# Kernel optimization log

Hardware: AMD Instinct MI355X
Metric: run time of the kernel (lower is better)

The kernel has to match this reference:

```python
import jax, jax.numpy as jnp
import numpy as np

WS = (7, 7)          # window size
SS = (3, 3)          # shift size
HP, WP = 112, 112    # patch grid H, W
C = 128              # embedding dim
NH = 8               # heads
HD = C // NH
SCALE = HD ** -0.5
N = WS[0] * WS[1]    # tokens per window = 49
B = 32


def _rel_index():
    ch = np.arange(WS[0]); cw = np.arange(WS[1])
    coords = np.stack(np.meshgrid(ch, cw, indexing='ij')).reshape(2, -1)
    rel = coords[:, :, None] - coords[:, None, :]
    rel = rel.transpose(1, 2, 0).copy()
    rel[..., 0] += WS[0] - 1
    rel[..., 1] += WS[1] - 1
    rel[..., 0] *= 2 * WS[1] - 1
    return rel.sum(-1)  # [N, N] int


def _attn_mask():
    img = np.zeros((HP, WP))
    hs = [slice(0, -WS[0]), slice(-WS[0], -SS[0]), slice(-SS[0], None)]
    ws = [slice(0, -WS[1]), slice(-WS[1], -SS[1]), slice(-SS[1], None)]
    cnt = 0
    for h in hs:
        for w in ws:
            img[h, w] = cnt
            cnt += 1
    mw = img.reshape(HP // WS[0], WS[0], WP // WS[1], WS[1]).transpose(0, 2, 1, 3).reshape(-1, N)
    am = mw[:, None, :] - mw[:, :, None]
    return np.where(am != 0, -100.0, 0.0).astype(np.float32)  # [nW, N, N]


REL_IDX = jnp.asarray(_rel_index())
ATTN_MASK = jnp.asarray(_attn_mask())


def _window_partition(x):
    b, h, w, c = x.shape
    x = x.reshape(b, h // WS[0], WS[0], w // WS[1], WS[1], c)
    return x.transpose(0, 1, 3, 2, 4, 5).reshape(-1, N, c)


def _window_reverse(win, h, w):
    c = win.shape[-1]
    x = win.reshape(-1, h // WS[0], w // WS[1], WS[0], WS[1], c)
    return x.transpose(0, 1, 3, 2, 4, 5).reshape(-1, h, w, c)


def _layernorm(x, w, b):
    mu = x.mean(-1, keepdims=True)
    var = x.var(-1, keepdims=True)
    return (x - mu) / jnp.sqrt(var + 1e-5) * w + b


def setup_inputs() -> dict:
    key = jax.random.key(0)
    ks = jax.random.split(key, 8)
    s = 0.02
    return {
        'x': jax.random.normal(ks[0], (B, HP, WP, C), jnp.float32),
        'qkv_w': jax.random.normal(ks[1], (C, 3 * C), jnp.float32) * s,
        'qkv_b': jnp.zeros((3 * C,), jnp.float32),
        'proj_w': jax.random.normal(ks[2], (C, C), jnp.float32) * s,
        'proj_b': jnp.zeros((C,), jnp.float32),
        'rpb': jax.random.normal(ks[3], ((2 * WS[0] - 1) * (2 * WS[1] - 1), NH), jnp.float32) * s,
        'ln1_w': jnp.ones((C,), jnp.float32),
        'ln1_b': jnp.zeros((C,), jnp.float32),
        'ln2_w': jnp.ones((C,), jnp.float32),
        'ln2_b': jnp.zeros((C,), jnp.float32),
        'w1': jax.random.normal(ks[4], (C, 4 * C), jnp.float32) * s,
        'b1': jnp.zeros((4 * C,), jnp.float32),
        'w2': jax.random.normal(ks[5], (4 * C, C), jnp.float32) * s,
        'b2': jnp.zeros((C,), jnp.float32),
    }


def reference(x, qkv_w, qkv_b, proj_w, proj_b, rpb, ln1_w, ln1_b, ln2_w, ln2_b, w1, b1, w2, b2):
    b, h, w, c = x.shape
    # NOTE: original code overwrites x with norm1(x), so the residual uses the
    # normed tensor -- reproduced faithfully here.
    xn = _layernorm(x, ln1_w, ln1_b)
    shifted = jnp.roll(xn, (-SS[0], -SS[1]), axis=(1, 2))
    xw = _window_partition(shifted)                      # [B*nW, N, C]
    qkv = xw @ qkv_w + qkv_b                             # [B*nW, N, 3C]
    qkv = qkv.reshape(-1, N, 3, NH, HD).transpose(2, 0, 3, 1, 4)
    q, k, v = qkv[0], qkv[1], qkv[2]                     # [B*nW, NH, N, HD]
    attn = jnp.einsum('bhnd,bhmd->bhnm', q * SCALE, k)   # [B*nW, NH, N, N]
    bias = rpb[REL_IDX].transpose(2, 0, 1)               # [NH, N, N]
    attn = attn + bias[None]
    n_w = ATTN_MASK.shape[0]
    attn = attn.reshape(b, n_w, NH, N, N) + ATTN_MASK[None, :, None]
    attn = jax.nn.softmax(attn.reshape(-1, NH, N, N), axis=-1)
    out = jnp.einsum('bhnm,bhmd->bhnd', attn, v)
    out = out.transpose(0, 2, 1, 3).reshape(-1, N, c)
    out = out @ proj_w + proj_b
    shifted = _window_reverse(out, h, w)
    shifted = jnp.roll(shifted, (SS[0], SS[1]), axis=(1, 2))
    y = xn + shifted
    hid = _layernorm(y, ln2_w, ln2_b)
    hid = jax.nn.gelu(hid @ w1 + b1) @ w2 + b2
    return y + hid
```

## Files before the change

### kernel.cpp

```cpp
#include <hip/hip_runtime.h>
#include <hip/hip_bf16.h>

#define DI __device__ __forceinline__

typedef unsigned short u16;
typedef unsigned int   u32;
typedef float  f32x4  __attribute__((ext_vector_type(4)));
typedef __bf16 bf16x8 __attribute__((ext_vector_type(8)));
typedef u16    us8    __attribute__((ext_vector_type(8)));

DI u16 f2bf(float f){
  u32 u = __builtin_bit_cast(u32, f);
  u = (u + 0x7fffu + ((u >> 16) & 1u)) >> 16;
  return (u16)u;
}
DI float bf2f(u16 h){
  u32 u = ((u32)h) << 16;
  return __builtin_bit_cast(float, u);
}

DI f32x4 mfma16(bf16x8 a, bf16x8 b, f32x4 c){
  return __builtin_amdgcn_mfma_f32_16x16x32_bf16(a, b, c, 0, 0, 0);
}
DI bf16x8 bzero(){
  us8 z = {0,0,0,0,0,0,0,0};
  return __builtin_bit_cast(bf16x8, z);
}
DI bf16x8 ld8s(const u16* p){ return *(const bf16x8*)p; }

__global__ void prep_kernel(const float* __restrict__ qkv_w, const float* __restrict__ proj_w,
                            const float* __restrict__ w1,    const float* __restrict__ w2,
                            const float* __restrict__ rpb,
                            u16* __restrict__ qkvwT, u16* __restrict__ projwT,
                            u16* __restrict__ w1T,   u16* __restrict__ w2T,
                            float* __restrict__ biasC)
{
  const int idx = blockIdx.x * blockDim.x + threadIdx.x;
  const int stride = gridDim.x * blockDim.x;
  for (int i = idx; i < 384*128; i += stride){ int o = i >> 7, k = i & 127; qkvwT[i] = f2bf(qkv_w[k*384 + o]); }
  for (int i = idx; i < 128*128; i += stride){ int o = i >> 7, k = i & 127; projwT[i] = f2bf(proj_w[k*128 + o]); }
  for (int i = idx; i < 512*128; i += stride){ int o = i >> 7, k = i & 127; w1T[i] = f2bf(w1[k*512 + o]); }
  for (int i = idx; i < 128*512; i += stride){ int o = i >> 9, k = i & 511; w2T[i] = f2bf(w2[k*128 + o]); }
  for (int i = idx; i < 4*8*64*64; i += stride){
    const int cls = i >> 15;
    const int rem = i & 32767;
    const int h = rem >> 12;
    const int km = rem & 4095;
    const int key = km >> 6, q = km & 63;
    float v;
    if (key >= 49) v = -1e30f;
    else if (q >= 49) v = 0.f;
    else {
      const int rel = (q/7 - key/7 + 6)*13 + (q%7 - key%7 + 6);
      v = rpb[rel*8 + h];
      const int rhF = cls >> 1, rwF = cls & 1;
      const int labq = (rhF ? ((q/7)   < 4 ? 1 : 2) : 0)*3 + (rwF ? ((q%7)   < 4 ? 1 : 2) : 0);
      const int labk = (rhF ? ((key/7) < 4 ? 1 : 2) : 0)*3 + (rwF ? ((key%7) < 4 ? 1 : 2) : 0);
      if (labq != labk) v -= 100.f;
    }
    biasC[i] = v;
  }
}

__global__ __launch_bounds__(256, 3) void attn_kernel(
    const float* __restrict__ x,
    const float* __restrict__ ln1w, const float* __restrict__ ln1b,
    const float* __restrict__ qkv_b, const float* __restrict__ proj_b,
    const u16* __restrict__ qkvwT, const u16* __restrict__ projwT,
    const float* __restrict__ biasC,
    float* __restrict__ y)
{
  __shared__ u16 qkPool[2*64*136];
  __shared__ u16 pool[128*72];

  u16* qB = qkPool;
  u16* kB = qkPool + 64*136;
  u16* xw = pool;
  float* aoS = (float*)qkPool;

  const int tid = threadIdx.x;
  const int lane = tid & 63;
  const int wv = tid >> 6;
  const int l15 = lane & 15;
  const int lq  = lane >> 4;
  const int blk = blockIdx.x;
  const int b  = blk >> 8;
  const int wi = blk & 255;
  const int wh = wi >> 4, ww = wi & 15;
  const int cls = ((wh == 15) ? 2 : 0) + ((ww == 15) ? 1 : 0);
  const int t = tid >> 2, g = tid & 3;

  u32 xnp[16];

  {
    float vals[32];
    float sum = 0.f, sq = 0.f;
    if (t < 49){
      const int r = t / 7, c = t % 7;
      const int hs   = (wh*7 + r + 3) % 112;
      const int wsrc = (ww*7 + c + 3) % 112;
      const float* src = x + ((size_t)((b*112 + hs)*112 + wsrc))*128 + g*32;
      #pragma unroll
      for (int j = 0; j < 8; j++){
        f32x4 v4 = *(const f32x4*)(src + 4*j);
        vals[4*j+0]=v4[0]; vals[4*j+1]=v4[1]; vals[4*j+2]=v4[2]; vals[4*j+3]=v4[3];
        sum += v4[0] + v4[1] + v4[2] + v4[3];
        sq  += v4[0]*v4[0] + v4[1]*v4[1] + v4[2]*v4[2] + v4[3]*v4[3];
      }
    } else {
      #pragma unroll
      for (int j = 0; j < 32; j++) vals[j] = 0.f;
    }
    sum += __shfl_xor(sum, 1); sum += __shfl_xor(sum, 2);
    sq  += __shfl_xor(sq, 1);  sq  += __shfl_xor(sq, 2);
    const float mu = sum * (1.f/128.f);
    const float var = sq * (1.f/128.f) - mu*mu;
    const float rs = rsqrtf(var + 1e-5f);
    #pragma unroll
    for (int j = 0; j < 32; j++){
      const int ch = g*32 + j;
      float xn = 0.f;
      if (t < 49) xn = (vals[j] - mu) * rs * ln1w[ch] + ln1b[ch];
      const u16 h = f2bf(xn);
      xw[(t*128 + ch) ^ ((t & 7) << 3)] = h;
      if (j & 1) xnp[j >> 1] |= ((u32)h << 16);
      else       xnp[j >> 1]  = (u32)h;
    }
  }
  __syncthreads();

  {
    const f32x4 fz = {0.f,0.f,0.f,0.f};
    f32x4 acc[4][6];
    #pragma unroll
    for (int mt = 0; mt < 4; mt++)
      #pragma unroll
      for (int nt = 0; nt < 6; nt++) acc[mt][nt] = fz;

    const int col0 = wv * 96;
    bf16x8 bbv[6];
    #pragma unroll
    for (int nt = 0; nt < 6; nt++)
      bbv[nt] = *(const bf16x8*)(qkvwT + (col0 + nt*16 + l15)*128 + (lq << 3));
    #pragma unroll
    for (int kk = 0; kk < 4; kk++){
      const int k0 = kk*32 + (lq << 3);
      bf16x8 a[4];
      #pragma unroll
      for (int mt = 0; mt < 4; mt++){
        const int row = mt*16 + l15;
        a[mt] = ld8s(&xw[(row*128 + k0) ^ ((row & 7) << 3)]);
      }
      bf16x8 bbn[6];
      if (kk < 3){
        const int k1 = (kk+1)*32 + (lq << 3);
        #pragma unroll
        for (int nt = 0; nt < 6; nt++)
          bbn[nt] = *(const bf16x8*)(qkvwT + (col0 + nt*16 + l15)*128 + k1);
      }
      __builtin_amdgcn_s_setprio(1);
      #pragma unroll
      for (int nt = 0; nt < 6; nt++)
        #pragma unroll
        for (int mt = 0; mt < 4; mt++)
          acc[mt][nt] = mfma16(a[mt], bbv[nt], acc[mt][nt]);
      __builtin_amdgcn_s_setprio(0);
      if (kk < 3){
        #pragma unroll
        for (int nt = 0; nt < 6; nt++) bbv[nt] = bbn[nt];
      }
    }
    __syncthreads();
    #pragma unroll
    for (int nt = 0; nt < 6; nt++){
      const int o = col0 + nt*16 + l15;
      const int which = o >> 7;
      const int ch = o & 127;
      const float bias = qkv_b[o];
      #pragma unroll
      for (int mt = 0; mt < 4; mt++){
        #pragma unroll
        for (int r = 0; r < 4; r++){
          const int tok = mt*16 + (lq << 2) + r;
          const float v = acc[mt][nt][r] + bias;
          if (which == 0)      qB[tok*136 + ch] = f2bf(v * 0.25f);
          else if (which == 1) kB[tok*136 + ch] = f2bf(v);
          else                 pool[ch*72 + tok] = f2bf(v);
        }
      }
    }
  }
  __syncthreads();

  {
    const f32x4 fz = {0.f,0.f,0.f,0.f};
    const int iq = wv*16 + l15;
    const float* bC = biasC + cls*32768 + iq;
    #pragma unroll 1
    for (int hb = 0; hb < 2; hb++){
      float p[4][4][4];
      #pragma unroll
      for (int hh = 0; hh < 4; hh++){
        const int h = hb*4 + hh;
        const bf16x8 bq = (lq < 2) ? ld8s(&qB[iq*136 + h*16 + (lq << 3)]) : bzero();
        const float* bh = bC + h*4096;
        __builtin_amdgcn_s_setprio(1);
        #pragma unroll
        for (int nt = 0; nt < 4; nt++){
          const int keyb = nt*16 + (lq << 2);
          f32x4 cf;
          cf[0] = bh[(keyb+0)*64];
          cf[1] = bh[(keyb+1)*64];
          cf[2] = bh[(keyb+2)*64];
          cf[3] = bh[(keyb+3)*64];
          const bf16x8 ak = (lq < 2) ? ld8s(&kB[(nt*16 + l15)*136 + h*16 + (lq << 3)]) : bzero();
          const f32x4 s4 = mfma16(ak, bq, cf);
          #pragma unroll
          for (int r = 0; r < 4; r++) p[hh][nt][r] = s4[r];
        }
        __builtin_amdgcn_s_setprio(0);
      }
      #pragma unroll
      for (int hh = 0; hh < 4; hh++){
        float m = -3e38f;
        #pragma unroll
        for (int nt = 0; nt < 4; nt++)
          #pragma unroll
          for (int r = 0; r < 4; r++) m = fmaxf(m, p[hh][nt][r]);
        m = fmaxf(m, __shfl_xor(m, 16));
        m = fmaxf(m, __shfl_xor(m, 32));
        float sum = 0.f;
        #pragma unroll
        for (int nt = 0; nt < 4; nt++)
          #pragma unroll
          for (int r = 0; r < 4; r++){
            const float e = __expf(p[hh][nt][r] - m);
            p[hh][nt][r] = e;
            sum += e;
          }
        sum += __shfl_xor(sum, 16);
        sum += __shfl_xor(sum, 32);
        const float inv = 1.f / sum;
        #pragma unroll
        for (int nt = 0; nt < 4; nt++)
          #pragma unroll
          for (int r = 0; r < 4; r++) p[hh][nt][r] *= inv;
      }
      f32x4 oaccb[4];
      #pragma unroll
      for (int hh = 0; hh < 4; hh++){
        const int h = hb*4 + hh;
        bf16x8 pa[2];
        #pragma unroll
        for (int kk = 0; kk < 2; kk++){
          us8 tmp;
          #pragma unroll
          for (int j = 0; j < 8; j++){
            const int srcLane = ((((lq << 1) + (j >> 2)) & 3) << 4) + l15;
            const float va = __shfl(p[hh][2*kk    ][j & 3], srcLane);
            const float vb = __shfl(p[hh][2*kk + 1][j & 3], srcLane);
            tmp[j] = f2bf((lq & 2) ? vb : va);
          }
          pa[kk] = __builtin_bit_cast(bf16x8, tmp);
        }
        f32x4 oacc = fz;
        __builtin_amdgcn_s_setprio(1);
        #pragma unroll
        for (int kk = 0; kk < 2; kk++){
          const bf16x8 bv = ld8s(&pool[(h*16 + l15)*72 + kk*32 + (lq << 3)]);
          oacc = mfma16(pa[kk], bv, oacc);
        }
        __builtin_amdgcn_s_setprio(0);
        oaccb[hh] = oacc;
      }
      __syncthreads();
      #pragma unroll
      for (int hh = 0; hh < 4; hh++){
        const int h = hb*4 + hh;
        #pragma unroll
        for (int r = 0; r < 4; r++){
          const int tok = wv*16 + (lq << 2) + r;
          kB[tok*136 + h*16 + l15] = f2bf(oaccb[hh][r]);
        }
      }
    }
  }
  __syncthreads();

  {
    const f32x4 fz = {0.f,0.f,0.f,0.f};
    bf16x8 pw[4][2];
    #pragma unroll
    for (int kk = 0; kk < 4; kk++){
      const int k0 = kk*32 + (lq << 3);
      #pragma unroll
      for (int nt = 0; nt < 2; nt++)
        pw[kk][nt] = *(const bf16x8*)(projwT + (wv*32 + nt*16 + l15)*128 + k0);
    }
    f32x4 acc[4][2];
    #pragma unroll
    for (int mt = 0; mt < 4; mt++){ acc[mt][0] = fz; acc[mt][1] = fz; }
    #pragma unroll
    for (int kk = 0; kk < 4; kk++){
      const int k0 = kk*32 + (lq << 3);
      bf16x8 a[4];
      #pragma unroll
      for (int mt = 0; mt < 4; mt++){
        const int row = mt*16 + l15;
        a[mt] = ld8s(&kB[row*136 + k0]);
      }
      __builtin_amdgcn_s_setprio(1);
      #pragma unroll
      for (int nt = 0; nt < 2; nt++)
        #pragma unroll
        for (int mt = 0; mt < 4; mt++)
          acc[mt][nt] = mfma16(a[mt], pw[kk][nt], acc[mt][nt]);
      __builtin_amdgcn_s_setprio(0);
    }
    __syncthreads();
    #pragma unroll
    for (int nt = 0; nt < 2; nt++){
      const int ch = wv*32 + nt*16 + l15;
      const float pb = proj_b[ch];
      #pragma unroll
      for (int mt = 0; mt < 4; mt++){
        #pragma unroll
        for (int r = 0; r < 4; r++){
          const int tok = mt*16 + (lq << 2) + r;
          aoS[(tok*128 + ch) ^ ((tok & 7) << 2)] = acc[mt][nt][r] + pb;
        }
      }
    }
  }
  __syncthreads();

  if (t < 49){
    const int rr = t / 7, cc = t % 7;
    const int hs   = (wh*7 + rr + 3) % 112;
    const int wsrc = (ww*7 + cc + 3) % 112;
    float* dst = y + ((size_t)((b*112 + hs)*112 + wsrc))*128 + g*32;
    #pragma unroll
    for (int j = 0; j < 8; j++){
      const int idx = (t*128 + g*32 + 4*j) ^ ((t & 7) << 2);
      const f32x4 a4 = *(const f32x4*)(aoS + idx);
      f32x4 o4;
      #pragma unroll
      for (int e = 0; e < 4; e++){
        const int c = 4*j + e;
        const u16 h = (u16)(xnp[c >> 1] >> ((c & 1) * 16));
        o4[e] = bf2f(h) + a4[e];
      }
      *(f32x4*)(dst + 4*j) = o4;
    }
  }
}

__global__ __launch_bounds__(256, 2) void mlp_kernel(
    const float* __restrict__ ln2w, const float* __restrict__ ln2b,
    const float* __restrict__ b1, const float* __restrict__ b2,
    const u16* __restrict__ w1T, const u16* __restrict__ w2T,
    float* __restrict__ y)
{
  __shared__ u16 yn[128*128];
  __shared__ u16 hid[128*128];
  const int tid = threadIdx.x;
  const int lane = tid & 63;
  const int wv = tid >> 6;
  const int l15 = lane & 15;
  const int lq  = lane >> 4;
  const size_t base = (size_t)blockIdx.x * 128;
  const f32x4 fz = {0.f,0.f,0.f,0.f};

  {
    const int t2 = tid >> 1, gh = tid & 1;
    const float* src = y + (base + t2)*128 + gh*64;
    float vals[64];
    float sum = 0.f, sq = 0.f;
    #pragma unroll
    for (int j = 0; j < 16; j++){
      f32x4 v4 = *(const f32x4*)(src + 4*j);
      vals[4*j+0]=v4[0]; vals[4*j+1]=v4[1]; vals[4*j+2]=v4[2]; vals[4*j+3]=v4[3];
      sum += v4[0] + v4[1] + v4[2] + v4[3];
      sq  += v4[0]*v4[0] + v4[1]*v4[1] + v4[2]*v4[2] + v4[3]*v4[3];
    }
    sum += __shfl_xor(sum, 1);
    sq  += __shfl_xor(sq, 1);
    const float mu = sum * (1.f/128.f);
    const float rs = rsqrtf(sq * (1.f/128.f) - mu*mu + 1e-5f);
    #pragma unroll
    for (int j = 0; j < 64; j++){
      const int ch = gh*64 + j;
      yn[(t2*128 + ch) ^ ((t2 & 7) << 3)] = f2bf((vals[j] - mu) * rs * ln2w[ch] + ln2b[ch]);
    }
  }
  __syncthreads();

  f32x4 acc2[8][2];
  #pragma unroll
  for (int mt = 0; mt < 8; mt++){ acc2[mt][0] = fz; acc2[mt][1] = fz; }

  #pragma unroll 1
  for (int pass = 0; pass < 4; pass++){
    bf16x8 bb1[4][2];
    #pragma unroll
    for (int kk = 0; kk < 4; kk++){
      const int k0 = kk*32 + (lq << 3);
      #pragma unroll
      for (int nt = 0; nt < 2; nt++){
        const int o = pass*128 + wv*32 + nt*16 + l15;
        bb1[kk][nt] = *(const bf16x8*)(w1T + o*128 + k0);
      }
    }
    f32x4 acc[8][2];
    #pragma unroll
    for (int mt = 0; mt < 8; mt++){ acc[mt][0] = fz; acc[mt][1] = fz; }
    #pragma unroll
    for (int kk = 0; kk < 4; kk++){
      const int k0 = kk*32 + (lq << 3);
      bf16x8 a[8];
      #pragma unroll
      for (int mt = 0; mt < 8; mt++){
        const int row = mt*16 + l15;
        a[mt] = ld8s(&yn[(row*128 + k0) ^ ((row & 7) << 3)]);
      }
      #pragma unroll
      for (int nt = 0; nt < 2; nt++)
        #pragma unroll
        for (int mt = 0; mt < 8; mt++)
          acc[mt][nt] = mfma16(a[mt], bb1[kk][nt], acc[mt][nt]);
    }
    bf16x8 bb2[4][2];
    #pragma unroll
    for (int kk = 0; kk < 4; kk++){
      const int k0 = kk*32 + (lq << 3);
      #pragma unroll
      for (int nt = 0; nt < 2; nt++){
        const int o = wv*32 + nt*16 + l15;
        bb2[kk][nt] = *(const bf16x8*)(w2T + o*512 + pass*128 + k0);
      }
    }
    if (pass > 0) __syncthreads();
    #pragma unroll
    for (int nt = 0; nt < 2; nt++){
      const int o = pass*128 + wv*32 + nt*16 + l15;
      const int cl = wv*32 + nt*16 + l15;
      const float bb1s = b1[o];
      #pragma unroll
      for (int mt = 0; mt < 8; mt++){
        #pragma unroll
        for (int r = 0; r < 4; r++){
          const int tok = mt*16 + (lq << 2) + r;
          const float v = acc[mt][nt][r] + bb1s;
          const float u = 0.7978845608028654f * (v + 0.044715f * v*v*v);
          const float th = 1.f - 2.f / (__expf(2.f*u) + 1.f);
          const float gel = 0.5f * v * (1.f + th);
          hid[(tok*128 + cl) ^ ((tok & 7) << 3)] = f2bf(gel);
        }
      }
    }
    __syncthreads();

    #pragma unroll
    for (int kk = 0; kk < 4; kk++){
      const int k0 = kk*32 + (lq << 3);
      bf16x8 a[8];
      #pragma unroll
      for (int mt = 0; mt < 8; mt++){
        const int row = mt*16 + l15;
        a[mt] = ld8s(&hid[(row*128 + k0) ^ ((row & 7) << 3)]);
      }
      #pragma unroll
      for (int nt = 0; nt < 2; nt++)
        #pragma unroll
        for (int mt = 0; mt < 8; mt++)
          acc2[mt][nt] = mfma16(a[mt], bb2[kk][nt], acc2[mt][nt]);
    }
  }

  #pragma unroll
  for (int nt = 0; nt < 2; nt++){
    const int ch = wv*32 + nt*16 + l15;
    const float bb2s = b2[ch];
    #pragma unroll
    for (int mt = 0; mt < 8; mt++){
      #pragma unroll
      for (int r = 0; r < 4; r++){
        const int tok = mt*16 + (lq << 2) + r;
        const size_t gi = (base + tok)*128 + ch;
        y[gi] = y[gi] + acc2[mt][nt][r] + bb2s;
      }
    }
  }
}

extern "C" void kernel_launch(void* const* d_in, const int* in_sizes, int n_in,
                              void* d_out, int out_size, void* d_ws, size_t ws_size,
                              hipStream_t stream)
{
  const float* x      = (const float*)d_in[0];
  const float* qkv_w  = (const float*)d_in[1];
  const float* qkv_b  = (const float*)d_in[2];
  const float* proj_w = (const float*)d_in[3];
  const float* proj_b = (const float*)d_in[4];
  const float* rpb    = (const float*)d_in[5];
  const float* ln1w   = (const float*)d_in[6];
  const float* ln1b   = (const float*)d_in[7];
  const float* ln2w   = (const float*)d_in[8];
  const float* ln2b   = (const float*)d_in[9];
  const float* w1     = (const float*)d_in[10];
  const float* b1     = (const float*)d_in[11];
  const float* w2     = (const float*)d_in[12];
  const float* b2     = (const float*)d_in[13];

  char* ws = (char*)d_ws;
  u16*   qkvwT  = (u16*)(ws + 0);
  u16*   projwT = (u16*)(ws + 98304);
  u16*   w1T    = (u16*)(ws + 131072);
  u16*   w2T    = (u16*)(ws + 262144);
  float* biasC  = (float*)(ws + 393216);
  float* y = (float*)d_out;

  prep_kernel<<<512, 256, 0, stream>>>(qkv_w, proj_w, w1, w2, rpb,
                                       qkvwT, projwT, w1T, w2T, biasC);
  attn_kernel<<<8192, 256, 0, stream>>>(x, ln1w, ln1b, qkv_b, proj_b,
                                        qkvwT, projwT, biasC, y);
  mlp_kernel<<<3136, 256, 0, stream>>>(ln2w, ln2b, b1, b2, w1T, w2T, y);
}
```

Before: 1.143 ms.

## Fuse MLP into attention kernel to avoid global round-trip of y

Merges the separate MLP kernel into the per-window attention kernel. The residual y, its LayerNorm, the two MLP GEMMs and the final residual add now run on the 64-row window tile held in shared memory, and y and the MLP output are kept in bf16 LDS buffers. This removes one launch and the write plus re-read of the full fp32 y tensor. In exchange, MLP work is padded from 49 to 64 rows per window, intermediate precision drops to bf16, and the s_setprio hints are removed.

```diff
diff --git a/kernel.cpp b/kernel.cpp
--- a/kernel.cpp
+++ b/kernel.cpp
@@ -62,13 +62,16 @@
   }
 }
 
-__global__ __launch_bounds__(256, 3) void attn_kernel(
+__global__ __launch_bounds__(256, 3) void fused_kernel(
     const float* __restrict__ x,
     const float* __restrict__ ln1w, const float* __restrict__ ln1b,
     const float* __restrict__ qkv_b, const float* __restrict__ proj_b,
+    const float* __restrict__ ln2w, const float* __restrict__ ln2b,
+    const float* __restrict__ b1, const float* __restrict__ b2,
     const u16* __restrict__ qkvwT, const u16* __restrict__ projwT,
+    const u16* __restrict__ w1T, const u16* __restrict__ w2T,
     const float* __restrict__ biasC,
-    float* __restrict__ y)
+    float* __restrict__ out)
 {
   __shared__ u16 qkPool[2*64*136];
   __shared__ u16 pool[128*72];
@@ -77,6 +80,9 @@
   u16* kB = qkPool + 64*136;
   u16* xw = pool;
   float* aoS = (float*)qkPool;
+  u16* yB   = qkPool;
+  u16* hidL = qkPool + 8704;
+  u16* ynL  = pool;
 
   const int tid = threadIdx.x;
   const int lane = tid & 63;
@@ -89,6 +95,7 @@
   const int wh = wi >> 4, ww = wi & 15;
   const int cls = ((wh == 15) ? 2 : 0) + ((ww == 15) ? 1 : 0);
   const int t = tid >> 2, g = tid & 3;
+  const f32x4 fz = {0.f,0.f,0.f,0.f};
 
   u32 xnp[16];
 
@@ -130,7 +137,6 @@
   __syncthreads();
 
   {
-    const f32x4 fz = {0.f,0.f,0.f,0.f};
     f32x4 acc[4][6];
     #pragma unroll
     for (int mt = 0; mt < 4; mt++)
@@ -158,13 +164,11 @@
         for (int nt = 0; nt < 6; nt++)
           bbn[nt] = *(const bf16x8*)(qkvwT + (col0 + nt*16 + l15)*128 + k1);
       }
-      __builtin_amdgcn_s_setprio(1);
       #pragma unroll
       for (int nt = 0; nt < 6; nt++)
         #pragma unroll
         for (int mt = 0; mt < 4; mt++)
           acc[mt][nt] = mfma16(a[mt], bbv[nt], acc[mt][nt]);
-      __builtin_amdgcn_s_setprio(0);
       if (kk < 3){
         #pragma unroll
         for (int nt = 0; nt < 6; nt++) bbv[nt] = bbn[nt];
@@ -193,7 +197,6 @@
   __syncthreads();
 
   {
-    const f32x4 fz = {0.f,0.f,0.f,0.f};
     const int iq = wv*16 + l15;
     const float* bC = biasC + cls*32768 + iq;
     #pragma unroll 1
@@ -204,7 +207,6 @@
         const int h = hb*4 + hh;
         const bf16x8 bq = (lq < 2) ? ld8s(&qB[iq*136 + h*16 + (lq << 3)]) : bzero();
         const float* bh = bC + h*4096;
-        __builtin_amdgcn_s_setprio(1);
         #pragma unroll
         for (int nt = 0; nt < 4; nt++){
           const int keyb = nt*16 + (lq << 2);
@@ -218,7 +220,6 @@
           #pragma unroll
           for (int r = 0; r < 4; r++) p[hh][nt][r] = s4[r];
         }
-        __builtin_amdgcn_s_setprio(0);
       }
       #pragma unroll
       for (int hh = 0; hh < 4; hh++){
@@ -264,13 +265,11 @@
           pa[kk] = __builtin_bit_cast(bf16x8, tmp);
         }
         f32x4 oacc = fz;
-        __builtin_amdgcn_s_setprio(1);
         #pragma unroll
         for (int kk = 0; kk < 2; kk++){
           const bf16x8 bv = ld8s(&pool[(h*16 + l15)*72 + kk*32 + (lq << 3)]);
           oacc = mfma16(pa[kk], bv, oacc);
         }
-        __builtin_amdgcn_s_setprio(0);
         oaccb[hh] = oacc;
       }
       __syncthreads();
@@ -288,7 +287,6 @@
   __syncthreads();
 
   {
-    const f32x4 fz = {0.f,0.f,0.f,0.f};
     bf16x8 pw[4][2];
     #pragma unroll
     for (int kk = 0; kk < 4; kk++){
@@ -309,13 +307,11 @@
         const int row = mt*16 + l15;
         a[mt] = ld8s(&kB[row*136 + k0]);
       }
-      __builtin_amdgcn_s_setprio(1);
       #pragma unroll
       for (int nt = 0; nt < 2; nt++)
         #pragma unroll
         for (int mt = 0; mt < 4; mt++)
           acc[mt][nt] = mfma16(a[mt], pw[kk][nt], acc[mt][nt]);
-      __builtin_amdgcn_s_setprio(0);
     }
     __syncthreads();
     #pragma unroll
@@ -334,70 +330,35 @@
   }
   __syncthreads();
 
-  if (t < 49){
-    const int rr = t / 7, cc = t % 7;
-    const int hs   = (wh*7 + rr + 3) % 112;
-    const int wsrc = (ww*7 + cc + 3) % 112;
-    float* dst = y + ((size_t)((b*112 + hs)*112 + wsrc))*128 + g*32;
-    #pragma unroll
-    for (int j = 0; j < 8; j++){
-      const int idx = (t*128 + g*32 + 4*j) ^ ((t & 7) << 2);
-      const f32x4 a4 = *(const f32x4*)(aoS + idx);
-      f32x4 o4;
-      #pragma unroll
-      for (int e = 0; e < 4; e++){
-        const int c = 4*j + e;
-        const u16 h = (u16)(xnp[c >> 1] >> ((c & 1) * 16));
-        o4[e] = bf2f(h) + a4[e];
-      }
-      *(f32x4*)(dst + 4*j) = o4;
-    }
-  }
-}
-
-__global__ __launch_bounds__(256, 2) void mlp_kernel(
-    const float* __restrict__ ln2w, const float* __restrict__ ln2b,
-    const float* __restrict__ b1, const float* __restrict__ b2,
-    const u16* __restrict__ w1T, const u16* __restrict__ w2T,
-    float* __restrict__ y)
-{
-  __shared__ u16 yn[128*128];
-  __shared__ u16 hid[128*128];
-  const int tid = threadIdx.x;
-  const int lane = tid & 63;
-  const int wv = tid >> 6;
-  const int l15 = lane & 15;
-  const int lq  = lane >> 4;
-  const size_t base = (size_t)blockIdx.x * 128;
-  const f32x4 fz = {0.f,0.f,0.f,0.f};
-
   {
-    const int t2 = tid >> 1, gh = tid & 1;
-    const float* src = y + (base + t2)*128 + gh*64;
-    float vals[64];
+    float yv[32];
     float sum = 0.f, sq = 0.f;
     #pragma unroll
-    for (int j = 0; j < 16; j++){
-      f32x4 v4 = *(const f32x4*)(src + 4*j);
-      vals[4*j+0]=v4[0]; vals[4*j+1]=v4[1]; vals[4*j+2]=v4[2]; vals[4*j+3]=v4[3];
-      sum += v4[0] + v4[1] + v4[2] + v4[3];
-      sq  += v4[0]*v4[0] + v4[1]*v4[1] + v4[2]*v4[2] + v4[3]*v4[3];
-    }
-    sum += __shfl_xor(sum, 1);
-    sq  += __shfl_xor(sq, 1);
+    for (int j = 0; j < 32; j++){
+      const int idx = (t*128 + g*32 + j) ^ ((t & 7) << 2);
+      const u16 h = (u16)(xnp[j >> 1] >> ((j & 1) * 16));
+      yv[j] = bf2f(h) + aoS[idx];
+      sum += yv[j];
+      sq  += yv[j]*yv[j];
+    }
+    __syncthreads();
+    sum += __shfl_xor(sum, 1); sum += __shfl_xor(sum, 2);
+    sq  += __shfl_xor(sq, 1);  sq  += __shfl_xor(sq, 2);
     const float mu = sum * (1.f/128.f);
     const float rs = rsqrtf(sq * (1.f/128.f) - mu*mu + 1e-5f);
     #pragma unroll
-    for (int j = 0; j < 64; j++){
-      const int ch = gh*64 + j;
-      yn[(t2*128 + ch) ^ ((t2 & 7) << 3)] = f2bf((vals[j] - mu) * rs * ln2w[ch] + ln2b[ch]);
-    }
-  }
-  __syncthreads();
-
-  f32x4 acc2[8][2];
+    for (int j = 0; j < 32; j++){
+      const int ch = g*32 + j;
+      const int sidx = (t*128 + ch) ^ ((t & 7) << 3);
+      yB[sidx]  = f2bf(yv[j]);
+      ynL[sidx] = f2bf((yv[j] - mu) * rs * ln2w[ch] + ln2b[ch]);
+    }
+  }
+  __syncthreads();
+
+  f32x4 acc2[4][2];
   #pragma unroll
-  for (int mt = 0; mt < 8; mt++){ acc2[mt][0] = fz; acc2[mt][1] = fz; }
+  for (int mt = 0; mt < 4; mt++){ acc2[mt][0] = fz; acc2[mt][1] = fz; }
 
   #pragma unroll 1
   for (int pass = 0; pass < 4; pass++){
@@ -411,33 +372,23 @@
         bb1[kk][nt] = *(const bf16x8*)(w1T + o*128 + k0);
       }
     }
-    f32x4 acc[8][2];
-    #pragma unroll
-    for (int mt = 0; mt < 8; mt++){ acc[mt][0] = fz; acc[mt][1] = fz; }
+    f32x4 acc[4][2];
+    #pragma unroll
+    for (int mt = 0; mt < 4; mt++){ acc[mt][0] = fz; acc[mt][1] = fz; }
     #pragma unroll
     for (int kk = 0; kk < 4; kk++){
       const int k0 = kk*32 + (lq << 3);
-      bf16x8 a[8];
-      #pragma unroll
-      for (int mt = 0; mt < 8; mt++){
+      bf16x8 a[4];
+      #pragma unroll
+      for (int mt = 0; mt < 4; mt++){
         const int row = mt*16 + l15;
-        a[mt] = ld8s(&yn[(row*128 + k0) ^ ((row & 7) << 3)]);
+        a[mt] = ld8s(&ynL[(row*128 + k0) ^ ((row & 7) << 3)]);
       }
       #pragma unroll
       for (int nt = 0; nt < 2; nt++)
         #pragma unroll
-        for (int mt = 0; mt < 8; mt++)
+        for (int mt = 0; mt < 4; mt++)
           acc[mt][nt] = mfma16(a[mt], bb1[kk][nt], acc[mt][nt]);
-    }
-    bf16x8 bb2[4][2];
-    #pragma unroll
-    for (int kk = 0; kk < 4; kk++){
-      const int k0 = kk*32 + (lq << 3);
-      #pragma unroll
-      for (int nt = 0; nt < 2; nt++){
-        const int o = wv*32 + nt*16 + l15;
-        bb2[kk][nt] = *(const bf16x8*)(w2T + o*512 + pass*128 + k0);
-      }
     }
     if (pass > 0) __syncthreads();
     #pragma unroll
@@ -446,7 +397,7 @@
       const int cl = wv*32 + nt*16 + l15;
       const float bb1s = b1[o];
       #pragma unroll
-      for (int mt = 0; mt < 8; mt++){
+      for (int mt = 0; mt < 4; mt++){
         #pragma unroll
         for (int r = 0; r < 4; r++){
           const int tok = mt*16 + (lq << 2) + r;
@@ -454,41 +405,62 @@
           const float u = 0.7978845608028654f * (v + 0.044715f * v*v*v);
           const float th = 1.f - 2.f / (__expf(2.f*u) + 1.f);
           const float gel = 0.5f * v * (1.f + th);
-          hid[(tok*128 + cl) ^ ((tok & 7) << 3)] = f2bf(gel);
+          hidL[(tok*128 + cl) ^ ((tok & 7) << 3)] = f2bf(gel);
         }
       }
     }
     __syncthreads();
-
     #pragma unroll
     for (int kk = 0; kk < 4; kk++){
       const int k0 = kk*32 + (lq << 3);
-      bf16x8 a[8];
-      #pragma unroll
-      for (int mt = 0; mt < 8; mt++){
+      bf16x8 a[4];
+      #pragma unroll
+      for (int mt = 0; mt < 4; mt++){
         const int row = mt*16 + l15;
-        a[mt] = ld8s(&hid[(row*128 + k0) ^ ((row & 7) << 3)]);
-      }
-      #pragma unroll
-      for (int nt = 0; nt < 2; nt++)
-        #pragma unroll
-        for (int mt = 0; mt < 8; mt++)
-          acc2[mt][nt] = mfma16(a[mt], bb2[kk][nt], acc2[mt][nt]);
-    }
-  }
+        a[mt] = ld8s(&hidL[(row*128 + k0) ^ ((row & 7) << 3)]);
+      }
+      #pragma unroll
+      for (int nt = 0; nt < 2; nt++){
+        const int o = wv*32 + nt*16 + l15;
+        const bf16x8 bb = *(const bf16x8*)(w2T + o*512 + pass*128 + k0);
+        #pragma unroll
+        for (int mt = 0; mt < 4; mt++)
+          acc2[mt][nt] = mfma16(a[mt], bb, acc2[mt][nt]);
+      }
+    }
+  }
+  __syncthreads();
 
   #pragma unroll
   for (int nt = 0; nt < 2; nt++){
     const int ch = wv*32 + nt*16 + l15;
     const float bb2s = b2[ch];
     #pragma unroll
-    for (int mt = 0; mt < 8; mt++){
+    for (int mt = 0; mt < 4; mt++){
       #pragma unroll
       for (int r = 0; r < 4; r++){
         const int tok = mt*16 + (lq << 2) + r;
-        const size_t gi = (base + tok)*128 + ch;
-        y[gi] = y[gi] + acc2[mt][nt][r] + bb2s;
-      }
+        hidL[(tok*128 + ch) ^ ((tok & 7) << 3)] = f2bf(acc2[mt][nt][r] + bb2s);
+      }
+    }
+  }
+  __syncthreads();
+
+  if (t < 49){
+    const int rr = t / 7, cc = t % 7;
+    const int hs   = (wh*7 + rr + 3) % 112;
+    const int wsrc = (ww*7 + cc + 3) % 112;
+    float* dst = out + ((size_t)((b*112 + hs)*112 + wsrc))*128 + g*32;
+    #pragma unroll
+    for (int j = 0; j < 8; j++){
+      f32x4 o4;
+      #pragma unroll
+      for (int e = 0; e < 4; e++){
+        const int ch = g*32 + 4*j + e;
+        const int sidx = (t*128 + ch) ^ ((t & 7) << 3);
+        o4[e] = bf2f(yB[sidx]) + bf2f(hidL[sidx]);
+      }
+      *(f32x4*)(dst + 4*j) = o4;
     }
   }
 }
@@ -518,11 +490,11 @@
   u16*   w1T    = (u16*)(ws + 131072);
   u16*   w2T    = (u16*)(ws + 262144);
   float* biasC  = (float*)(ws + 393216);
-  float* y = (float*)d_out;
+  float* out = (float*)d_out;
 
   prep_kernel<<<512, 256, 0, stream>>>(qkv_w, proj_w, w1, w2, rpb,
                                        qkvwT, projwT, w1T, w2T, biasC);
-  attn_kernel<<<8192, 256, 0, stream>>>(x, ln1w, ln1b, qkv_b, proj_b,
-                                        qkvwT, projwT, biasC, y);
-  mlp_kernel<<<3136, 256, 0, stream>>>(ln2w, ln2b, b1, b2, w1T, w2T, y);
-}
+  fused_kernel<<<8192, 256, 0, stream>>>(x, ln1w, ln1b, qkv_b, proj_b,
+                                         ln2w, ln2b, b1, b2,
+                                         qkvwT, projwT, w1T, w2T, biasC, out);
+}
```

After: 1.187 ms. +3.9%, slower.
